# Performance work log

Hardware: AMD Instinct MI355X
Metric: run time of the kernel (lower is better)

Reference implementation:

```python
import jax, jax.numpy as jnp
import numpy as np

T = 2048      # number of utterances in the dialogue (sequential loop dim)
L = 50        # tokens per utterance
V = 30000     # vocab size
D = 300       # word embedding dim
NF = 64       # CNN filters per width
H = 100       # hidden size (hard-coded in CMN)
NC = 7        # emotion classes
WIND = 40     # args.wind1 sliding memory window
HOPS = 3      # args.hops
NEG = -1e10   # masked_fill value in dotprod_attention


def setup_inputs() -> dict:
    key = jax.random.key(0)
    ks = jax.random.split(key, 24)
    s = 0.05

    def n(k, shape):
        return jax.random.normal(k, shape, jnp.float32) * s

    return {
        "sents": jax.random.randint(ks[0], (T, L), 0, V, dtype=jnp.int32),
        "lengths": jax.random.randint(ks[1], (T,), 1, L, dtype=jnp.int32),
        "emb": n(ks[2], (V, D)),
        "Wc3": n(ks[3], (NF, 1, 3, D)), "bc3": n(ks[4], (NF,)),
        "Wc4": n(ks[5], (NF, 1, 4, D)), "bc4": n(ks[6], (NF,)),
        "Wc5": n(ks[7], (NF, 1, 5, D)), "bc5": n(ks[8], (NF,)),
        "Wt": n(ks[9], (3 * NF, H)), "bt": n(ks[10], (H,)),
        "Wih_c": n(ks[11], (3 * H, H)), "Whh_c": n(ks[12], (3 * H, H)),
        "bih_c": n(ks[13], (3 * H,)), "bhh_c": n(ks[14], (3 * H,)),
        "Wih_m": n(ks[15], (3 * H, H)), "Whh_m": n(ks[16], (3 * H, H)),
        "bih_m": n(ks[17], (3 * H,)), "bhh_m": n(ks[18], (3 * H,)),
        "Wcls": n(ks[19], (H, NC)), "bcls": n(ks[20], (NC,)),
    }


def _gru_cell(x, h, Wih, Whh, bih, bhh):
    # torch GRU cell, gate order (r, z, n)
    gi = x @ Wih.T + bih
    gh = h @ Whh.T + bhh
    ir, iz, inn = jnp.split(gi, 3, axis=-1)
    hr, hz, hn = jnp.split(gh, 3, axis=-1)
    r = jax.nn.sigmoid(ir + hr)
    z = jax.nn.sigmoid(iz + hz)
    nw = jnp.tanh(inn + r * hn)
    return (1.0 - z) * nw + z * h


def reference(sents, lengths, emb, Wc3, bc3, Wc4, bc4, Wc5, bc5, Wt, bt,
              Wih_c, Whh_c, bih_c, bhh_c, Wih_m, Whh_m, bih_m, bhh_m,
              Wcls, bcls):
    # ---- CNN utterance encoder (dropout layers are identity in eval) ----
    w = emb[sents]                       # (T, L, D)
    x = w[:, None]                       # (T, 1, L, D)  NCHW
    feats = []
    for Wc, bc in ((Wc3, bc3), (Wc4, bc4), (Wc5, bc5)):
        y = jax.lax.conv_general_dilated(
            x, Wc, window_strides=(1, 1), padding='VALID',
            dimension_numbers=('NCHW', 'OIHW', 'NCHW'))  # (T, NF, L-fs+1, 1)
        feats.append(jnp.max(jax.nn.relu(y + bc[None, :, None, None]), axis=(2, 3)))
    s_utt = jnp.tanh(jnp.concatenate(feats, axis=1) @ Wt + bt)  # (T, H)

    # ---- context GRU over utterances 0..T-2 (hidden after torch step i is hiddens[i-1]) ----
    def cont_step(h, u):
        h2 = _gru_cell(u, h, Wih_c, Whh_c, bih_c, bhh_c)
        return h2, h2
    _, hiddens = jax.lax.scan(cont_step, jnp.zeros((H,), jnp.float32), s_utt[:-1])  # (T-1, H)

    # ---- sliding memory windows: step i (1..T-1) sees hiddens[i-WIND .. i-1], newest last ----
    idx = jnp.arange(1, T)[:, None] - WIND + jnp.arange(WIND)[None, :]  # (T-1, WIND)
    valid = idx >= 0
    mem_all = jnp.where(valid[..., None], hiddens[jnp.clip(idx, 0)], 0.0)  # (T-1, WIND, H)

    def attend(query, mem, v):
        # query: (H,), mem: (WIND, H), v: (WIND,) bool
        for _ in range(HOPS):
            scores = jnp.where(v, mem @ query, NEG)
            a = jax.nn.softmax(scores)
            query = jnp.tanh(query + a @ mem)
            if HOPS > 1:
                # mem_gru over the valid suffix of the window (zero init hidden,
                # padded slots skipped so recurrence starts at first valid slot)
                def mstep(hm, xv):
                    xx, vv = xv
                    hn = _gru_cell(xx, hm, Wih_m, Whh_m, bih_m, bhh_m)
                    hm = jnp.where(vv, hn, hm)
                    return hm, hm
                _, mem = jax.lax.scan(mstep, jnp.zeros((H,), jnp.float32), (mem, v))
        return query

    queries = jax.vmap(attend)(s_utt[1:], mem_all, valid)       # (T-1, H)
    s_cont = jnp.concatenate([s_utt[:1], queries], axis=0)      # (T, H)
    logits = s_cont @ Wcls + bcls                                # (T, NC)
    return jax.nn.log_softmax(logits, axis=1)
```

## Files before the change

kernel.cpp:

```cpp
#include <hip/hip_runtime.h>

#define TT 2048
#define LL 50
#define DD 300
#define HH 100
#define NCC 7

typedef unsigned short u16;
typedef unsigned int u32;
typedef _Float16 f16x2 __attribute__((ext_vector_type(2)));
typedef _Float16 f16x4 __attribute__((ext_vector_type(4)));
typedef _Float16 f16x8 __attribute__((ext_vector_type(8)));
typedef float f32x4 __attribute__((ext_vector_type(4)));

__device__ __forceinline__ float frcp(float x){ return __builtin_amdgcn_rcpf(x); }
__device__ __forceinline__ float sigm(float x){ return frcp(1.f + __expf(-x)); }
__device__ __forceinline__ float ftanh(float x){ return 1.f - 2.f * frcp(1.f + __expf(2.f * x)); }

#if defined(__has_builtin)
#if __has_builtin(__builtin_amdgcn_fdot2)
#define HAS_FDOT2 1
#endif
#endif
__device__ __forceinline__ float fdot2(f16x2 a, f16x2 b, float c){
#ifdef HAS_FDOT2
  return __builtin_amdgcn_fdot2(a, b, c, false);
#else
  return c + (float)a.x * (float)b.x + (float)a.y * (float)b.y;
#endif
}
__device__ __forceinline__ f16x2 pk(float x, float y){ f16x2 r; r.x = (_Float16)x; r.y = (_Float16)y; return r; }

__global__ __launch_bounds__(256) void k_prep(const float* __restrict__ Wc3,
    const float* __restrict__ Wc4, const float* __restrict__ Wc5, _Float16* __restrict__ wtp)
{
  const int t = blockIdx.x;
  int kki, ntile, kt;
  if (t < 120){ kki = 0; ntile = t / 30;        kt = t % 30; }
  else if (t < 280){ kki = 1; int r = t - 120; ntile = r / 40; kt = r % 40; }
  else { kki = 2; int r = t - 280;             ntile = r / 50; kt = r % 50; }
  const float* W = (kki == 0) ? Wc3 : ((kki == 1) ? Wc4 : Wc5);
  const int kk = 3 + kki;
  #pragma unroll
  for (int u = 0; u < 2; ++u){
    int e = threadIdx.x * 2 + u;
    int lane = e >> 3, i = e & 7;
    int k = kt * 32 + (lane >> 4) * 8 + i;
    int f = ntile * 16 + (lane & 15);
    int j = k / 320, d = k - j * 320;
    float v = (d < DD) ? W[((size_t)f * kk + j) * DD + d] : 0.f;
    wtp[(size_t)t * 512 + e] = (_Float16)v;
  }
}

__global__ __launch_bounds__(256) void k_prep2(const float* __restrict__ Whh,
    const float* __restrict__ Wih, _Float16* __restrict__ wpkW, _Float16* __restrict__ wpkI)
{
  const float* W = (blockIdx.x == 0) ? Whh : Wih;
  _Float16* dst  = (blockIdx.x == 0) ? wpkW : wpkI;
  for (int idx = threadIdx.x; idx < 28 * 4 * 64 * 8; idx += 256){
    int i = idx & 7, lane = (idx >> 3) & 63, kt = (idx >> 9) & 3, mt = idx >> 11;
    int rl = lane & 15, gp = lane >> 4;
    int p = mt * 16 + rl;
    int k = kt * 32 + gp * 8 + i;
    int uu = p >> 2, g = p & 3;
    float v = (mt < 25 && g < 3 && k < 100) ? W[(size_t)(uu + 100 * g) * 100 + k] : 0.f;
    dst[idx] = (_Float16)v;
  }
}

#define WST 328
__global__ __launch_bounds__(256) void k_cnn(const int* __restrict__ sents,
    const float* __restrict__ emb, const _Float16* __restrict__ wtp,
    const float* __restrict__ bc3, const float* __restrict__ bc4, const float* __restrict__ bc5,
    const float* __restrict__ Wt,  const float* __restrict__ bt,
    float* __restrict__ su)
{
  __shared__ __attribute__((aligned(16))) _Float16 w16[52 * WST];
  __shared__ float feats[192];
  __shared__ int ids[LL];
  const int tid = threadIdx.x;
  const int s = blockIdx.x;

  if (tid < LL) ids[tid] = sents[s * LL + tid];
  for (int e = tid; e < 52 * WST / 2; e += 256) ((u32*)w16)[e] = 0u;
  __syncthreads();
  for (int e = tid; e < LL * 75; e += 256){
    int l = e / 75, d4 = (e - l * 75) * 4;
    float4 v = *(const float4*)&emb[(size_t)ids[l] * DD + d4];
    _Float16* p = &w16[l * WST + d4];
    p[0] = (_Float16)v.x; p[1] = (_Float16)v.y; p[2] = (_Float16)v.z; p[3] = (_Float16)v.w;
  }
  __syncthreads();

  const int lane = tid & 63, wid = tid >> 6;
  const int rl = lane & 15, gp = lane >> 4;
  const int kkstart[3] = {0, 120, 280};
  float fmaxv[3];
  #pragma unroll
  for (int kki = 0; kki < 3; ++kki){
    const int kk = 3 + kki, nkt = kk * 10, Pk = LL - kk + 1;
    f32x4 acc0 = {0.f,0.f,0.f,0.f}, acc1 = acc0, acc2 = acc0;
    const f16x8* bp = (const f16x8*)(wtp + (size_t)(kkstart[kki] + wid * nkt) * 512) + lane;
    int j = 0, d = gp * 8;
    for (int kt = 0; kt < nkt; ++kt){
      f16x8 b  = bp[(size_t)kt * 64];
      f16x8 a0 = *(const f16x8*)&w16[(rl      + j) * WST + d];
      f16x8 a1 = *(const f16x8*)&w16[(16 + rl + j) * WST + d];
      f16x8 a2 = *(const f16x8*)&w16[(32 + rl + j) * WST + d];
      acc0 = __builtin_amdgcn_mfma_f32_16x16x32_f16(a0, b, acc0, 0, 0, 0);
      acc1 = __builtin_amdgcn_mfma_f32_16x16x32_f16(a1, b, acc1, 0, 0, 0);
      acc2 = __builtin_amdgcn_mfma_f32_16x16x32_f16(a2, b, acc2, 0, 0, 0);
      d += 32; if (d >= 320){ d -= 320; ++j; }
    }
    float m = -1e30f;
    #pragma unroll
    for (int r = 0; r < 4; ++r){
      int p0 = gp * 4 + r;
      if (p0 < Pk)      m = fmaxf(m, acc0[r]);
      if (16 + p0 < Pk) m = fmaxf(m, acc1[r]);
      if (32 + p0 < Pk) m = fmaxf(m, acc2[r]);
    }
    m = fmaxf(m, __shfl_xor(m, 16));
    m = fmaxf(m, __shfl_xor(m, 32));
    fmaxv[kki] = m;
  }
  if (lane < 16){
    feats[  0 + wid * 16 + lane] = fmaxv[0];
    feats[ 64 + wid * 16 + lane] = fmaxv[1];
    feats[128 + wid * 16 + lane] = fmaxv[2];
  }
  __syncthreads();
  if (tid < 192){
    float bias = (tid < 64) ? bc3[tid] : ((tid < 128) ? bc4[tid - 64] : bc5[tid - 128]);
    feats[tid] = fmaxf(0.f, feats[tid] + bias);
  }
  __syncthreads();
  if (tid < HH){
    float acc = bt[tid];
    for (int c = 0; c < 192; ++c)
      acc += feats[c] * Wt[c * HH + tid];
    su[(size_t)s * HH + tid] = ftanh(acc);
  }
}

__global__ __launch_bounds__(320) void k_gi(const float* __restrict__ src,
    const float* __restrict__ W, const float* __restrict__ b, float* __restrict__ dst)
{
  __shared__ float x[HH];
  const int t = blockIdx.x, tid = threadIdx.x;
  if (tid < HH) x[tid] = src[(size_t)t * HH + tid];
  __syncthreads();
  if (tid < 300){
    float acc = b[tid];
    const float* wr = W + (size_t)tid * HH;
    #pragma unroll
    for (int i = 0; i < 25; ++i){
      float4 wv = *(const float4*)(wr + 4 * i);
      float4 xv = *(const float4*)&x[4 * i];
      acc += xv.x * wv.x + xv.y * wv.y + xv.z * wv.z + xv.w * wv.w;
    }
    dst[(size_t)t * 300 + tid] = acc;
  }
}

#define CH 32
__global__ __launch_bounds__(320, 1) void k_scan(const float* __restrict__ gi,
    const float* __restrict__ Whh, const float* __restrict__ bhh,
    float* __restrict__ hid, int steps)
{
  __shared__ __attribute__((aligned(16))) _Float16 h16[128];
  __shared__ __attribute__((aligned(16))) float gh_l[304];
  __shared__ float gi_buf[CH * 300];
  __shared__ float hid_buf[CH * HH];
  const int tid = threadIdx.x;
  const int lane = tid & 63, wvid = tid >> 6;
  const int rl = lane & 15, gp = lane >> 4;

  f16x8 afrag[4][4];
  #pragma unroll
  for (int m = 0; m < 4; ++m){
    int mt = wvid + 5 * m;
    int row = mt * 16 + rl;
    #pragma unroll
    for (int kt = 0; kt < 4; ++kt){
      f16x8 f;
      #pragma unroll
      for (int i = 0; i < 8; ++i){
        int k = kt * 32 + gp * 8 + i;
        float v = (row < 300 && k < 100) ? Whh[(size_t)row * 100 + k] : 0.f;
        f[i] = (_Float16)v;
      }
      afrag[m][kt] = f;
    }
  }
  float bhr = 0.f, bhz = 0.f, bhn = 0.f, hreg = 0.f;
  if (tid < HH){ bhr = bhh[tid]; bhz = bhh[tid + 100]; bhn = bhh[tid + 200]; }
  if (tid < 128) h16[tid] = (_Float16)0.f;
  {
    int c0 = (steps < CH ? steps : CH) * 75;
    for (int e = tid; e < c0; e += 320)
      ((float4*)gi_buf)[e] = ((const float4*)gi)[e];
  }
  __syncthreads();

  int t0 = 0;
  while (t0 < steps){
    int cnt = steps - t0; if (cnt > CH) cnt = CH;
    for (int s = 0; s < cnt; ++s){
      {
        const f16x8* hp = (const f16x8*)h16;
        f16x8 bf0 = hp[ 0 + gp], bf1 = hp[ 4 + gp], bf2 = hp[ 8 + gp], bf3 = hp[12 + gp];
        #pragma unroll
        for (int m = 0; m < 4; ++m){
          f32x4 acc = {0.f, 0.f, 0.f, 0.f};
          acc = __builtin_amdgcn_mfma_f32_16x16x32_f16(afrag[m][0], bf0, acc, 0, 0, 0);
          acc = __builtin_amdgcn_mfma_f32_16x16x32_f16(afrag[m][1], bf1, acc, 0, 0, 0);
          acc = __builtin_amdgcn_mfma_f32_16x16x32_f16(afrag[m][2], bf2, acc, 0, 0, 0);
          acc = __builtin_amdgcn_mfma_f32_16x16x32_f16(afrag[m][3], bf3, acc, 0, 0, 0);
          int mt = wvid + 5 * m;
          if (rl == 0 && mt < 19)
            *(float4*)&gh_l[mt * 16 + gp * 4] = *(float4*)&acc;
        }
      }
      __syncthreads();
      if (tid < HH){
        const float* gpp = gi_buf + s * 300;
        float r = sigm(gpp[tid]       + gh_l[tid]       + bhr);
        float z = sigm(gpp[tid + 100] + gh_l[tid + 100] + bhz);
        float n = ftanh(gpp[tid + 200] + r * (gh_l[tid + 200] + bhn));
        float o = (1.f - z) * n + z * hreg;
        hreg = o;
        h16[tid] = (_Float16)o;
        hid_buf[s * HH + tid] = o;
      }
      __syncthreads();
    }
    for (int e = tid; e < cnt * 25; e += 320)
      ((float4*)(hid + (size_t)t0 * HH))[e] = ((const float4*)hid_buf)[e];
    int nt0 = t0 + cnt;
    int ncnt = steps - nt0; if (ncnt > CH) ncnt = CH; if (ncnt < 0) ncnt = 0;
    for (int e = tid; e < ncnt * 75; e += 320)
      ((float4*)gi_buf)[e] = ((const float4*)(gi + (size_t)nt0 * 300))[e];
    __syncthreads();
    t0 = nt0;
  }
}

__global__ __launch_bounds__(256, 1) void k_att2(
    const float* __restrict__ su, const float* __restrict__ hid, const float* __restrict__ gm,
    const _Float16* __restrict__ wpkW, const _Float16* __restrict__ wpkI,
    const float* __restrict__ bih, const float* __restrict__ bhh,
    float* __restrict__ scont)
{
  __shared__ __attribute__((aligned(16))) _Float16 MEM[40][8][136];
  __shared__ __attribute__((aligned(16))) _Float16 H16[2][8][136];
  __shared__ __attribute__((aligned(16))) _Float16 GI2[8][8][100][4];
  __shared__ float QL[8][104];
  __shared__ float SC[8][40];

  const int tid = threadIdx.x;
  const int lane = tid & 63, wvid = tid >> 6;
  const int rl = lane & 15, gp = lane >> 4;
  const int qbase = blockIdx.x * 8;
  const int j = rl & 7;
  const int qi = qbase + j;
  int wminj = 39 - qi; if (wminj < 0) wminj = 0;
  if (qi >= TT - 1) wminj = 40;

  f16x8 aW[7][4];
  #pragma unroll
  for (int t = 0; t < 7; ++t){
    int mt = wvid + 4 * t;
    #pragma unroll
    for (int kt = 0; kt < 4; ++kt)
      aW[t][kt] = *(const f16x8*)(wpkW + (size_t)((mt * 4 + kt) * 64 + lane) * 8);
  }
  float bi_[7][3];
  #pragma unroll
  for (int t = 0; t < 7; ++t){
    int mt = wvid + 4 * t;
    bool v = (mt < 25);
    int uu = v ? (mt * 4 + gp) : 0;
    bi_[t][0] = v ? bih[uu]       : 0.f;
    bi_[t][1] = v ? bih[uu + 100] : 0.f;
    bi_[t][2] = v ? bih[uu + 200] : 0.f;
  }
  const int cbase = (rl < 8) ? 0 : 4;
  float bh_[4][3]; int cu[4]; bool cv[4];
  #pragma unroll
  for (int tt = 0; tt < 4; ++tt){
    int t = cbase + tt;
    int mt = wvid + 4 * t;
    bool v = (t < 7) && (mt < 25);
    cv[tt] = v;
    int uu = v ? (mt * 4 + gp) : 0;
    cu[tt] = uu;
    bh_[tt][0] = v ? bhh[uu]       : 0.f;
    bh_[tt][1] = v ? bhh[uu + 100] : 0.f;
    bh_[tt][2] = v ? bhh[uu + 200] : 0.f;
  }

  for (int e = tid; e < 40 * 8 * 34; e += 256){
    int i4 = e % 34, wj = e / 34, w = wj >> 3, jj = wj & 7;
    int qq = qbase + jj;
    int row = qq - 39 + w;
    f16x4 v4 = {0, 0, 0, 0};
    if (i4 < 25 && qq < TT - 1 && row >= 0){
      float4 f = *(const float4*)&hid[(size_t)row * HH + i4 * 4];
      v4[0] = (_Float16)f.x; v4[1] = (_Float16)f.y; v4[2] = (_Float16)f.z; v4[3] = (_Float16)f.w;
    }
    *(f16x4*)&MEM[w][jj][i4 * 4] = v4;
  }
  for (int e = tid; e < 8 * 104; e += 256){
    int jj = e / 104, ii = e % 104;
    int qq = qbase + jj;
    QL[jj][ii] = (ii < 100 && qq < TT - 1) ? su[(size_t)(qq + 1) * HH + ii] : 0.f;
  }
  for (int e = tid; e < 2 * 8 * 136; e += 256) ((_Float16*)H16)[e] = (_Float16)0;
  __syncthreads();

  for (int hop = 0; hop < 3; ++hop){
    for (int e = tid; e < 320; e += 256){
      int jj = e / 40, w = e % 40;
      int qq = qbase + jj;
      int wm = 39 - qq; if (wm < 0) wm = 0; if (qq >= TT - 1) wm = 40;
      float acc = 0.f;
      if (w >= wm){
        #pragma unroll
        for (int g = 0; g < 13; ++g){
          f16x8 m8 = *(const f16x8*)&MEM[w][jj][g * 8];
          const float* qp = &QL[jj][g * 8];
          #pragma unroll
          for (int i = 0; i < 8; ++i) acc += (float)m8[i] * qp[i];
        }
        SC[jj][w] = acc;
      } else SC[jj][w] = -1e10f;
    }
    __syncthreads();
    if (tid < 8){
      float m = -3e38f;
      for (int w = 0; w < 40; ++w) m = fmaxf(m, SC[tid][w]);
      float s = 0.f;
      for (int w = 0; w < 40; ++w){ float e = __expf(SC[tid][w] - m); SC[tid][w] = e; s += e; }
      float inv = frcp(s);
      for (int w = 0; w < 40; ++w) SC[tid][w] *= inv;
    }
    __syncthreads();
    for (int e = tid; e < 400; e += 256){
      int jj = e / 50, i2 = e % 50;
      float c0 = 0.f, c1 = 0.f;
      for (int w = 0; w < 40; ++w){
        float a = SC[jj][w];
        f16x2 m2 = *(const f16x2*)&MEM[w][jj][i2 * 2];
        c0 += a * (float)m2.x; c1 += a * (float)m2.y;
      }
      float q0 = ftanh(QL[jj][i2 * 2]     + c0);
      float q1 = ftanh(QL[jj][i2 * 2 + 1] + c1);
      QL[jj][i2 * 2] = q0; QL[jj][i2 * 2 + 1] = q1;
      if (hop == 2){
        int qq = qbase + jj;
        if (qq < TT - 1)
          *(float2*)&scont[(size_t)(qq + 1) * HH + i2 * 2] = make_float2(q0, q1);
      }
    }
    if (hop == 2) break;
    for (int e = tid; e < 800; e += 256) H16[0][e / 100][e % 100] = (_Float16)0;
    float hrg[4] = {0.f, 0.f, 0.f, 0.f};
    __syncthreads();

    for (int c = 0; c < 5; ++c){
      if (hop == 0){
        for (int e = tid; e < 6400; e += 256){
          int s8 = e / 800, jj = (e / 100) & 7, uu = e % 100;
          int qq = qbase + jj;
          int row = qq - 39 + c * 8 + s8;
          f16x4 g4 = {0, 0, 0, 0};
          if (qq < TT - 1 && row >= 0){
            const float* gr = &gm[(size_t)row * 300];
            g4[0] = (_Float16)gr[uu]; g4[1] = (_Float16)gr[uu + 100]; g4[2] = (_Float16)gr[uu + 200];
          }
          *(f16x4*)&GI2[s8][jj][uu][0] = g4;
        }
      } else {
        #pragma unroll
        for (int nt = 0; nt < 4; ++nt){
          f16x8 bf[4];
          #pragma unroll
          for (int kt = 0; kt < 4; ++kt)
            bf[kt] = *(const f16x8*)&MEM[c * 8 + nt * 2 + (rl >> 3)][rl & 7][kt * 32 + gp * 8];
          #pragma unroll
          for (int t = 0; t < 7; ++t){
            int mt = wvid + 4 * t;
            if (mt < 25){
              f32x4 ac = {0.f, 0.f, 0.f, 0.f};
              #pragma unroll
              for (int kt = 0; kt < 4; ++kt){
                f16x8 ai = *(const f16x8*)(wpkI + (size_t)((mt * 4 + kt) * 64 + lane) * 8);
                ac = __builtin_amdgcn_mfma_f32_16x16x32_f16(ai, bf[kt], ac, 0, 0, 0);
              }
              int uu = mt * 4 + gp;
              int s8 = nt * 2 + (rl >> 3), jj = rl & 7;
              f16x4 g4;
              g4[0] = (_Float16)(ac[0] + bi_[t][0]);
              g4[1] = (_Float16)(ac[1] + bi_[t][1]);
              g4[2] = (_Float16)(ac[2] + bi_[t][2]);
              g4[3] = (_Float16)0.f;
              *(f16x4*)&GI2[s8][jj][uu][0] = g4;
            }
          }
        }
      }
      __syncthreads();
      for (int s = 0; s < 8; ++s){
        int w = c * 8 + s;
        const _Float16 (*hs)[136] = H16[w & 1];
        _Float16 (*hd)[136] = H16[(w + 1) & 1];
        f16x8 b0 = *(const f16x8*)&hs[j][      gp * 8];
        f16x8 b1 = *(const f16x8*)&hs[j][32  + gp * 8];
        f16x8 b2 = *(const f16x8*)&hs[j][64  + gp * 8];
        f16x8 b3 = *(const f16x8*)&hs[j][96  + gp * 8];
        f32x4 acc[7];
        #pragma unroll
        for (int t = 0; t < 7; ++t){
          int mt = wvid + 4 * t;
          f32x4 a = {0.f, 0.f, 0.f, 0.f};
          if (mt < 25){
            a = __builtin_amdgcn_mfma_f32_16x16x32_f16(aW[t][0], b0, a, 0, 0, 0);
            a = __builtin_amdgcn_mfma_f32_16x16x32_f16(aW[t][1], b1, a, 0, 0, 0);
            a = __builtin_amdgcn_mfma_f32_16x16x32_f16(aW[t][2], b2, a, 0, 0, 0);
            a = __builtin_amdgcn_mfma_f32_16x16x32_f16(aW[t][3], b3, a, 0, 0, 0);
          }
          acc[t] = a;
        }
        const bool vw = (w >= wminj);
        #pragma unroll
        for (int tt = 0; tt < 4; ++tt){
          if (cv[tt]){
            f32x4 ac = (rl < 8) ? acc[tt] : acc[(tt + 4 < 7) ? (tt + 4) : 6];
            f16x4 g4 = *(const f16x4*)&GI2[s][j][cu[tt]][0];
            float r = sigm((float)g4[0] + ac[0] + bh_[tt][0]);
            float z = sigm((float)g4[1] + ac[1] + bh_[tt][1]);
            float n = ftanh((float)g4[2] + r * (ac[2] + bh_[tt][2]));
            float o = vw ? ((1.f - z) * n + z * hrg[tt]) : hrg[tt];
            hrg[tt] = o;
            hd[j][cu[tt]]     = (_Float16)o;
            MEM[w][j][cu[tt]] = (_Float16)o;
          }
        }
        __syncthreads();
      }
    }
  }
}

__global__ __launch_bounds__(256) void k_cls(const float* __restrict__ su, const float* __restrict__ scont,
    const float* __restrict__ Wcls, const float* __restrict__ bcls, float* __restrict__ out)
{
  __shared__ float wl[HH * NCC];
  __shared__ float bl[NCC];
  const int tid = threadIdx.x;
  for (int e = tid; e < HH * NCC; e += 256) wl[e] = Wcls[e];
  if (tid < NCC) bl[tid] = bcls[tid];
  __syncthreads();
  int r = blockIdx.x * 256 + tid;
  if (r < TT){
    const float* v = (r == 0) ? su : (scont + (size_t)r * HH);
    float l[NCC];
    #pragma unroll
    for (int c = 0; c < NCC; ++c) l[c] = bl[c];
    for (int h = 0; h < HH; ++h){
      float x = v[h];
      #pragma unroll
      for (int c = 0; c < NCC; ++c) l[c] += x * wl[h * NCC + c];
    }
    float m = l[0];
    #pragma unroll
    for (int c = 1; c < NCC; ++c) m = fmaxf(m, l[c]);
    float ssum = 0.f;
    #pragma unroll
    for (int c = 0; c < NCC; ++c) ssum += __expf(l[c] - m);
    float lse = m + __logf(ssum);
    #pragma unroll
    for (int c = 0; c < NCC; ++c) out[(size_t)r * NCC + c] = l[c] - lse;
  }
}

extern "C" void kernel_launch(void* const* d_in, const int* in_sizes, int n_in,
                              void* d_out, int out_size, void* d_ws, size_t ws_size,
                              hipStream_t stream)
{
  const int* sents  = (const int*)d_in[0];
  const float* emb    = (const float*)d_in[2];
  const float* Wc3    = (const float*)d_in[3];  const float* bc3 = (const float*)d_in[4];
  const float* Wc4    = (const float*)d_in[5];  const float* bc4 = (const float*)d_in[6];
  const float* Wc5    = (const float*)d_in[7];  const float* bc5 = (const float*)d_in[8];
  const float* Wt     = (const float*)d_in[9];  const float* bt  = (const float*)d_in[10];
  const float* Wih_c  = (const float*)d_in[11]; const float* Whh_c = (const float*)d_in[12];
  const float* bih_c  = (const float*)d_in[13]; const float* bhh_c = (const float*)d_in[14];
  const float* Wih_m  = (const float*)d_in[15]; const float* Whh_m = (const float*)d_in[16];
  const float* bih_m  = (const float*)d_in[17]; const float* bhh_m = (const float*)d_in[18];
  const float* Wcls   = (const float*)d_in[19]; const float* bcls  = (const float*)d_in[20];

  float* ws    = (float*)d_ws;
  float* su    = ws;
  float* gic   = su  + 204800;
  float* hid   = gic + 614100;
  float* gm    = gic;
  float* scont = hid + 204700;
  _Float16* wtp  = (_Float16*)(scont + 204800);
  _Float16* wpkW = wtp + 245760;
  _Float16* wpkI = wpkW + 57344;

  k_prep <<<480,    256, 0, stream>>>(Wc3, Wc4, Wc5, wtp);
  k_prep2<<<2,      256, 0, stream>>>(Whh_m, Wih_m, wpkW, wpkI);
  k_cnn  <<<TT,     256, 0, stream>>>(sents, emb, wtp, bc3, bc4, bc5, Wt, bt, su);
  k_gi   <<<TT - 1, 320, 0, stream>>>(su, Wih_c, bih_c, gic);
  k_scan <<<1,      320, 0, stream>>>(gic, Whh_c, bhh_c, hid, TT - 1);
  k_gi   <<<TT - 1, 320, 0, stream>>>(hid, Wih_m, bih_m, gm);
  k_att2 <<<256,    256, 0, stream>>>(su, hid, gm, wpkW, wpkI, bih_m, bhh_m, scont);
  k_cls  <<<(TT + 255) / 256, 256, 0, stream>>>(su, scont, Wcls, bcls, (float*)d_out);
}
```

Baseline: 1.744 ms.

## Fuse CNN, GRU scan, attention and classifier into one persistent flag-synchronized kernel

Merges the CNN encoder, input-gate projection, sequential context GRU scan, memory attention and classifier into a single persistent kernel of 256 blocks. Block 0 runs the scan and consumes per-utterance flags published by the other blocks. Once the scan progress counter passes their queries, all blocks run attention. The attention's hop-0 input projection is now computed in-kernel with MFMA instead of a separate k_gi pass, and the classifier is folded into the attention tail. This is meant to overlap CNN work with the serial scan and remove launch and global round-trip costs, at the price of spin-wait synchronization and a dependency on all 256 blocks being co-resident.

```diff
diff --git a/kernel.cpp b/kernel.cpp
--- a/kernel.cpp
+++ b/kernel.cpp
@@ -17,19 +17,12 @@
 __device__ __forceinline__ float sigm(float x){ return frcp(1.f + __expf(-x)); }
 __device__ __forceinline__ float ftanh(float x){ return 1.f - 2.f * frcp(1.f + __expf(2.f * x)); }
 
-#if defined(__has_builtin)
-#if __has_builtin(__builtin_amdgcn_fdot2)
-#define HAS_FDOT2 1
-#endif
-#endif
-__device__ __forceinline__ float fdot2(f16x2 a, f16x2 b, float c){
-#ifdef HAS_FDOT2
-  return __builtin_amdgcn_fdot2(a, b, c, false);
-#else
-  return c + (float)a.x * (float)b.x + (float)a.y * (float)b.y;
-#endif
-}
-__device__ __forceinline__ f16x2 pk(float x, float y){ f16x2 r; r.x = (_Float16)x; r.y = (_Float16)y; return r; }
+__device__ __forceinline__ int ld_acq(int* p){
+  return __hip_atomic_load(p, __ATOMIC_ACQUIRE, __HIP_MEMORY_SCOPE_AGENT);
+}
+__device__ __forceinline__ void st_rel(int* p, int v){
+  __hip_atomic_store(p, v, __ATOMIC_RELEASE, __HIP_MEMORY_SCOPE_AGENT);
+}
 
 __global__ __launch_bounds__(256) void k_prep(const float* __restrict__ Wc3,
     const float* __restrict__ Wc4, const float* __restrict__ Wc5, _Float16* __restrict__ wtp)
@@ -69,200 +62,248 @@
   }
 }
 
+__global__ __launch_bounds__(256) void k_zero(int* __restrict__ flags)
+{
+  int i = blockIdx.x * 256 + threadIdx.x;
+  if (i < 2049) flags[i] = 0;
+}
+
 #define WST 328
-__global__ __launch_bounds__(256) void k_cnn(const int* __restrict__ sents,
-    const float* __restrict__ emb, const _Float16* __restrict__ wtp,
+#define CH 32
+__global__ __launch_bounds__(256, 1) void k_mega(
+    const int* __restrict__ sents, const float* __restrict__ emb, const _Float16* __restrict__ wtp,
     const float* __restrict__ bc3, const float* __restrict__ bc4, const float* __restrict__ bc5,
     const float* __restrict__ Wt,  const float* __restrict__ bt,
-    float* __restrict__ su)
+    const float* __restrict__ Wih_c, const float* __restrict__ bih_c,
+    const float* __restrict__ Whh_c, const float* __restrict__ bhh_c,
+    const _Float16* __restrict__ wpkW, const _Float16* __restrict__ wpkI,
+    const float* __restrict__ bih_m, const float* __restrict__ bhh_m,
+    const float* __restrict__ Wcls, const float* __restrict__ bcls,
+    float* __restrict__ su, float* __restrict__ gic, float* __restrict__ hid,
+    int* __restrict__ flags, float* __restrict__ out)
 {
-  __shared__ __attribute__((aligned(16))) _Float16 w16[52 * WST];
-  __shared__ float feats[192];
-  __shared__ int ids[LL];
+  __shared__ __attribute__((aligned(16))) char smem[147456];
   const int tid = threadIdx.x;
-  const int s = blockIdx.x;
-
-  if (tid < LL) ids[tid] = sents[s * LL + tid];
-  for (int e = tid; e < 52 * WST / 2; e += 256) ((u32*)w16)[e] = 0u;
-  __syncthreads();
-  for (int e = tid; e < LL * 75; e += 256){
-    int l = e / 75, d4 = (e - l * 75) * 4;
-    float4 v = *(const float4*)&emb[(size_t)ids[l] * DD + d4];
-    _Float16* p = &w16[l * WST + d4];
-    p[0] = (_Float16)v.x; p[1] = (_Float16)v.y; p[2] = (_Float16)v.z; p[3] = (_Float16)v.w;
-  }
-  __syncthreads();
-
-  const int lane = tid & 63, wid = tid >> 6;
-  const int rl = lane & 15, gp = lane >> 4;
-  const int kkstart[3] = {0, 120, 280};
-  float fmaxv[3];
-  #pragma unroll
-  for (int kki = 0; kki < 3; ++kki){
-    const int kk = 3 + kki, nkt = kk * 10, Pk = LL - kk + 1;
-    f32x4 acc0 = {0.f,0.f,0.f,0.f}, acc1 = acc0, acc2 = acc0;
-    const f16x8* bp = (const f16x8*)(wtp + (size_t)(kkstart[kki] + wid * nkt) * 512) + lane;
-    int j = 0, d = gp * 8;
-    for (int kt = 0; kt < nkt; ++kt){
-      f16x8 b  = bp[(size_t)kt * 64];
-      f16x8 a0 = *(const f16x8*)&w16[(rl      + j) * WST + d];
-      f16x8 a1 = *(const f16x8*)&w16[(16 + rl + j) * WST + d];
-      f16x8 a2 = *(const f16x8*)&w16[(32 + rl + j) * WST + d];
-      acc0 = __builtin_amdgcn_mfma_f32_16x16x32_f16(a0, b, acc0, 0, 0, 0);
-      acc1 = __builtin_amdgcn_mfma_f32_16x16x32_f16(a1, b, acc1, 0, 0, 0);
-      acc2 = __builtin_amdgcn_mfma_f32_16x16x32_f16(a2, b, acc2, 0, 0, 0);
-      d += 32; if (d >= 320){ d -= 320; ++j; }
-    }
-    float m = -1e30f;
-    #pragma unroll
-    for (int r = 0; r < 4; ++r){
-      int p0 = gp * 4 + r;
-      if (p0 < Pk)      m = fmaxf(m, acc0[r]);
-      if (16 + p0 < Pk) m = fmaxf(m, acc1[r]);
-      if (32 + p0 < Pk) m = fmaxf(m, acc2[r]);
-    }
-    m = fmaxf(m, __shfl_xor(m, 16));
-    m = fmaxf(m, __shfl_xor(m, 32));
-    fmaxv[kki] = m;
-  }
-  if (lane < 16){
-    feats[  0 + wid * 16 + lane] = fmaxv[0];
-    feats[ 64 + wid * 16 + lane] = fmaxv[1];
-    feats[128 + wid * 16 + lane] = fmaxv[2];
-  }
-  __syncthreads();
-  if (tid < 192){
-    float bias = (tid < 64) ? bc3[tid] : ((tid < 128) ? bc4[tid - 64] : bc5[tid - 128]);
-    feats[tid] = fmaxf(0.f, feats[tid] + bias);
-  }
-  __syncthreads();
-  if (tid < HH){
-    float acc = bt[tid];
-    for (int c = 0; c < 192; ++c)
-      acc += feats[c] * Wt[c * HH + tid];
-    su[(size_t)s * HH + tid] = ftanh(acc);
-  }
-}
-
-__global__ __launch_bounds__(320) void k_gi(const float* __restrict__ src,
-    const float* __restrict__ W, const float* __restrict__ b, float* __restrict__ dst)
-{
-  __shared__ float x[HH];
-  const int t = blockIdx.x, tid = threadIdx.x;
-  if (tid < HH) x[tid] = src[(size_t)t * HH + tid];
-  __syncthreads();
-  if (tid < 300){
-    float acc = b[tid];
-    const float* wr = W + (size_t)tid * HH;
-    #pragma unroll
-    for (int i = 0; i < 25; ++i){
-      float4 wv = *(const float4*)(wr + 4 * i);
-      float4 xv = *(const float4*)&x[4 * i];
-      acc += xv.x * wv.x + xv.y * wv.y + xv.z * wv.z + xv.w * wv.w;
-    }
-    dst[(size_t)t * 300 + tid] = acc;
-  }
-}
-
-#define CH 32
-__global__ __launch_bounds__(320, 1) void k_scan(const float* __restrict__ gi,
-    const float* __restrict__ Whh, const float* __restrict__ bhh,
-    float* __restrict__ hid, int steps)
-{
-  __shared__ __attribute__((aligned(16))) _Float16 h16[128];
-  __shared__ __attribute__((aligned(16))) float gh_l[304];
-  __shared__ float gi_buf[CH * 300];
-  __shared__ float hid_buf[CH * HH];
-  const int tid = threadIdx.x;
+  const int b = blockIdx.x;
   const int lane = tid & 63, wvid = tid >> 6;
   const int rl = lane & 15, gp = lane >> 4;
 
-  f16x8 afrag[4][4];
-  #pragma unroll
-  for (int m = 0; m < 4; ++m){
-    int mt = wvid + 5 * m;
-    int row = mt * 16 + rl;
+  if (b > 0){
+    _Float16* w16 = (_Float16*)smem;
+    float* feats  = (float*)(smem + 34112);
+    int*   ids    = (int*)(smem + 34880);
+    float* su_l   = (float*)(smem + 35088);
+
+    for (int s = b - 1; s < TT; s += 255){
+      if (tid < LL) ids[tid] = sents[s * LL + tid];
+      for (int e = tid; e < 52 * WST / 2; e += 256) ((u32*)w16)[e] = 0u;
+      __syncthreads();
+      for (int e = tid; e < LL * 75; e += 256){
+        int l = e / 75, d4 = (e - l * 75) * 4;
+        float4 v = *(const float4*)&emb[(size_t)ids[l] * DD + d4];
+        _Float16* p = &w16[l * WST + d4];
+        p[0] = (_Float16)v.x; p[1] = (_Float16)v.y; p[2] = (_Float16)v.z; p[3] = (_Float16)v.w;
+      }
+      __syncthreads();
+
+      const int kkstart[3] = {0, 120, 280};
+      float fmaxv[3];
+      #pragma unroll
+      for (int kki = 0; kki < 3; ++kki){
+        const int nkt = (3 + kki) * 10, Pk = LL - (3 + kki) + 1;
+        f32x4 acc0 = {0.f,0.f,0.f,0.f}, acc1 = acc0, acc2 = acc0;
+        const f16x8* bp = (const f16x8*)(wtp + (size_t)(kkstart[kki] + wvid * nkt) * 512) + lane;
+        int j = 0, d = gp * 8;
+        for (int kt = 0; kt < nkt; ++kt){
+          f16x8 bb = bp[(size_t)kt * 64];
+          f16x8 a0 = *(const f16x8*)&w16[(rl      + j) * WST + d];
+          f16x8 a1 = *(const f16x8*)&w16[(16 + rl + j) * WST + d];
+          f16x8 a2 = *(const f16x8*)&w16[(32 + rl + j) * WST + d];
+          acc0 = __builtin_amdgcn_mfma_f32_16x16x32_f16(a0, bb, acc0, 0, 0, 0);
+          acc1 = __builtin_amdgcn_mfma_f32_16x16x32_f16(a1, bb, acc1, 0, 0, 0);
+          acc2 = __builtin_amdgcn_mfma_f32_16x16x32_f16(a2, bb, acc2, 0, 0, 0);
+          d += 32; if (d >= 320){ d -= 320; ++j; }
+        }
+        float m = -1e30f;
+        #pragma unroll
+        for (int r = 0; r < 4; ++r){
+          int p0 = gp * 4 + r;
+          if (p0 < Pk)      m = fmaxf(m, acc0[r]);
+          if (16 + p0 < Pk) m = fmaxf(m, acc1[r]);
+          if (32 + p0 < Pk) m = fmaxf(m, acc2[r]);
+        }
+        m = fmaxf(m, __shfl_xor(m, 16));
+        m = fmaxf(m, __shfl_xor(m, 32));
+        fmaxv[kki] = m;
+      }
+      if (lane < 16){
+        feats[  0 + wvid * 16 + lane] = fmaxv[0];
+        feats[ 64 + wvid * 16 + lane] = fmaxv[1];
+        feats[128 + wvid * 16 + lane] = fmaxv[2];
+      }
+      __syncthreads();
+      if (tid < 192){
+        float bias = (tid < 64) ? bc3[tid] : ((tid < 128) ? bc4[tid - 64] : bc5[tid - 128]);
+        feats[tid] = fmaxf(0.f, feats[tid] + bias);
+      }
+      __syncthreads();
+      if (tid < HH){
+        float acc = bt[tid];
+        for (int c = 0; c < 192; ++c)
+          acc += feats[c] * Wt[c * HH + tid];
+        float v = ftanh(acc);
+        su[(size_t)s * HH + tid] = v;
+        su_l[tid] = v;
+      }
+      __syncthreads();
+      if (s < TT - 1){
+        for (int e = tid; e < 300; e += 256){
+          const float* wr = Wih_c + (size_t)e * 100;
+          float acc = bih_c[e];
+          #pragma unroll
+          for (int i = 0; i < 25; ++i){
+            float4 wv = *(const float4*)(wr + 4 * i);
+            float4 xv = *(const float4*)&su_l[4 * i];
+            acc += xv.x * wv.x + xv.y * wv.y + xv.z * wv.z + xv.w * wv.w;
+          }
+          gic[(size_t)s * 300 + e] = acc;
+        }
+      }
+      __syncthreads();
+      if (tid == 0){ __threadfence(); st_rel(&flags[s], 1); }
+    }
+  } else {
+    _Float16* h16  = (_Float16*)smem;
+    float* gh_l    = (float*)(smem + 256);
+    float* gi_buf  = (float*)(smem + 1472);
+    float* hid_buf = (float*)(smem + 39872);
+    const int steps = TT - 1;
+
+    f16x8 afrag[5][4];
     #pragma unroll
-    for (int kt = 0; kt < 4; ++kt){
-      f16x8 f;
+    for (int m = 0; m < 5; ++m){
+      int mt = wvid + 4 * m;
+      int row = mt * 16 + rl;
       #pragma unroll
-      for (int i = 0; i < 8; ++i){
-        int k = kt * 32 + gp * 8 + i;
-        float v = (row < 300 && k < 100) ? Whh[(size_t)row * 100 + k] : 0.f;
-        f[i] = (_Float16)v;
-      }
-      afrag[m][kt] = f;
-    }
-  }
-  float bhr = 0.f, bhz = 0.f, bhn = 0.f, hreg = 0.f;
-  if (tid < HH){ bhr = bhh[tid]; bhz = bhh[tid + 100]; bhn = bhh[tid + 200]; }
-  if (tid < 128) h16[tid] = (_Float16)0.f;
-  {
-    int c0 = (steps < CH ? steps : CH) * 75;
-    for (int e = tid; e < c0; e += 320)
-      ((float4*)gi_buf)[e] = ((const float4*)gi)[e];
-  }
+      for (int kt = 0; kt < 4; ++kt){
+        f16x8 f;
+        #pragma unroll
+        for (int i = 0; i < 8; ++i){
+          int k = kt * 32 + gp * 8 + i;
+          float v = (row < 300 && k < 100) ? Whh_c[(size_t)row * 100 + k] : 0.f;
+          f[i] = (_Float16)v;
+        }
+        afrag[m][kt] = f;
+      }
+    }
+    float bhr = 0.f, bhz = 0.f, bhn = 0.f, hreg = 0.f;
+    if (tid < HH){ bhr = bhh_c[tid]; bhz = bhh_c[tid + 100]; bhn = bhh_c[tid + 200]; }
+    if (tid < 128) h16[tid] = (_Float16)0.f;
+    {
+      int n0 = steps < CH ? steps : CH;
+      for (int e = tid; e < n0; e += 256)
+        while (!ld_acq(&flags[e])) __builtin_amdgcn_s_sleep(2);
+    }
+    __syncthreads();
+    {
+      int c0 = (steps < CH ? steps : CH) * 75;
+      for (int e = tid; e < c0; e += 256)
+        ((float4*)gi_buf)[e] = ((const float4*)gic)[e];
+    }
+    __syncthreads();
+
+    int t0 = 0;
+    while (t0 < steps){
+      int cnt = steps - t0; if (cnt > CH) cnt = CH;
+      for (int s = 0; s < cnt; ++s){
+        {
+          const f16x8* hp = (const f16x8*)h16;
+          f16x8 bf0 = hp[0 + gp], bf1 = hp[4 + gp], bf2 = hp[8 + gp], bf3 = hp[12 + gp];
+          #pragma unroll
+          for (int m = 0; m < 5; ++m){
+            f32x4 acc = {0.f, 0.f, 0.f, 0.f};
+            acc = __builtin_amdgcn_mfma_f32_16x16x32_f16(afrag[m][0], bf0, acc, 0, 0, 0);
+            acc = __builtin_amdgcn_mfma_f32_16x16x32_f16(afrag[m][1], bf1, acc, 0, 0, 0);
+            acc = __builtin_amdgcn_mfma_f32_16x16x32_f16(afrag[m][2], bf2, acc, 0, 0, 0);
+            acc = __builtin_amdgcn_mfma_f32_16x16x32_f16(afrag[m][3], bf3, acc, 0, 0, 0);
+            int mt = wvid + 4 * m;
+            if (rl == 0 && mt < 19)
+              *(float4*)&gh_l[mt * 16 + gp * 4] = *(float4*)&acc;
+          }
+        }
+        __syncthreads();
+        if (tid < HH){
+          const float* gpp = gi_buf + s * 300;
+          float r = sigm(gpp[tid]       + gh_l[tid]       + bhr);
+          float z = sigm(gpp[tid + 100] + gh_l[tid + 100] + bhz);
+          float n = ftanh(gpp[tid + 200] + r * (gh_l[tid + 200] + bhn));
+          float o = (1.f - z) * n + z * hreg;
+          hreg = o;
+          h16[tid] = (_Float16)o;
+          hid_buf[s * HH + tid] = o;
+        }
+        __syncthreads();
+      }
+      for (int e = tid; e < cnt * 25; e += 256)
+        ((float4*)(hid + (size_t)t0 * HH))[e] = ((const float4*)hid_buf)[e];
+      int nt0 = t0 + cnt;
+      int ncnt = steps - nt0; if (ncnt > CH) ncnt = CH; if (ncnt < 0) ncnt = 0;
+      for (int e = tid; e < ncnt; e += 256)
+        while (!ld_acq(&flags[nt0 + e])) __builtin_amdgcn_s_sleep(2);
+      __syncthreads();
+      if (tid == 0){ __threadfence(); st_rel(&flags[2048], nt0); }
+      for (int e = tid; e < ncnt * 75; e += 256)
+        ((float4*)gi_buf)[e] = ((const float4*)(gic + (size_t)nt0 * 300))[e];
+      __syncthreads();
+      t0 = nt0;
+    }
+  }
+
   __syncthreads();
-
-  int t0 = 0;
-  while (t0 < steps){
-    int cnt = steps - t0; if (cnt > CH) cnt = CH;
-    for (int s = 0; s < cnt; ++s){
-      {
-        const f16x8* hp = (const f16x8*)h16;
-        f16x8 bf0 = hp[ 0 + gp], bf1 = hp[ 4 + gp], bf2 = hp[ 8 + gp], bf3 = hp[12 + gp];
-        #pragma unroll
-        for (int m = 0; m < 4; ++m){
-          f32x4 acc = {0.f, 0.f, 0.f, 0.f};
-          acc = __builtin_amdgcn_mfma_f32_16x16x32_f16(afrag[m][0], bf0, acc, 0, 0, 0);
-          acc = __builtin_amdgcn_mfma_f32_16x16x32_f16(afrag[m][1], bf1, acc, 0, 0, 0);
-          acc = __builtin_amdgcn_mfma_f32_16x16x32_f16(afrag[m][2], bf2, acc, 0, 0, 0);
-          acc = __builtin_amdgcn_mfma_f32_16x16x32_f16(afrag[m][3], bf3, acc, 0, 0, 0);
-          int mt = wvid + 5 * m;
-          if (rl == 0 && mt < 19)
-            *(float4*)&gh_l[mt * 16 + gp * 4] = *(float4*)&acc;
-        }
-      }
-      __syncthreads();
-      if (tid < HH){
-        const float* gpp = gi_buf + s * 300;
-        float r = sigm(gpp[tid]       + gh_l[tid]       + bhr);
-        float z = sigm(gpp[tid + 100] + gh_l[tid + 100] + bhz);
-        float n = ftanh(gpp[tid + 200] + r * (gh_l[tid + 200] + bhn));
-        float o = (1.f - z) * n + z * hreg;
-        hreg = o;
-        h16[tid] = (_Float16)o;
-        hid_buf[s * HH + tid] = o;
-      }
-      __syncthreads();
-    }
-    for (int e = tid; e < cnt * 25; e += 320)
-      ((float4*)(hid + (size_t)t0 * HH))[e] = ((const float4*)hid_buf)[e];
-    int nt0 = t0 + cnt;
-    int ncnt = steps - nt0; if (ncnt > CH) ncnt = CH; if (ncnt < 0) ncnt = 0;
-    for (int e = tid; e < ncnt * 75; e += 320)
-      ((float4*)gi_buf)[e] = ((const float4*)(gi + (size_t)nt0 * 300))[e];
-    __syncthreads();
-    t0 = nt0;
-  }
-}
-
-__global__ __launch_bounds__(256, 1) void k_att2(
-    const float* __restrict__ su, const float* __restrict__ hid, const float* __restrict__ gm,
-    const _Float16* __restrict__ wpkW, const _Float16* __restrict__ wpkI,
-    const float* __restrict__ bih, const float* __restrict__ bhh,
-    float* __restrict__ scont)
-{
-  __shared__ __attribute__((aligned(16))) _Float16 MEM[40][8][136];
-  __shared__ __attribute__((aligned(16))) _Float16 H16[2][8][136];
-  __shared__ __attribute__((aligned(16))) _Float16 GI2[8][8][100][4];
-  __shared__ float QL[8][104];
-  __shared__ float SC[8][40];
-
-  const int tid = threadIdx.x;
-  const int lane = tid & 63, wvid = tid >> 6;
-  const int rl = lane & 15, gp = lane >> 4;
-  const int qbase = blockIdx.x * 8;
+  const int grp = (b == 0) ? 255 : (b - 1);
+  const int qbase = grp * 8;
+  if (tid < 8){
+    int qq = qbase + tid;
+    if (qq < TT - 1)
+      while (!ld_acq(&flags[qq + 1])) __builtin_amdgcn_s_sleep(8);
+  }
+  if (tid == 1){
+    int need = qbase + 8; if (need > TT - 1) need = TT - 1;
+    while (ld_acq(&flags[2048]) < need) __builtin_amdgcn_s_sleep(32);
+  }
+  if (b == 0 && tid == 0){
+    while (!ld_acq(&flags[0])) __builtin_amdgcn_s_sleep(2);
+    float l[NCC];
+    #pragma unroll
+    for (int c = 0; c < NCC; ++c) l[c] = bcls[c];
+    for (int h = 0; h < HH; ++h){
+      float x = su[h];
+      #pragma unroll
+      for (int c = 0; c < NCC; ++c) l[c] += x * Wcls[h * NCC + c];
+    }
+    float m = l[0];
+    #pragma unroll
+    for (int c = 1; c < NCC; ++c) m = fmaxf(m, l[c]);
+    float ssum = 0.f;
+    #pragma unroll
+    for (int c = 0; c < NCC; ++c) ssum += __expf(l[c] - m);
+    float lse = m + __logf(ssum);
+    #pragma unroll
+    for (int c = 0; c < NCC; ++c) out[c] = l[c] - lse;
+  }
+  __syncthreads();
+
+  _Float16* MEMb = (_Float16*)smem;
+  _Float16* H16b = (_Float16*)(smem + 87040);
+  _Float16* GI2b = (_Float16*)(smem + 91392);
+  float* QLb     = (float*)(smem + 142592);
+  float* SCb     = (float*)(smem + 145920);
+  #define MEM_(w,j,i)   MEMb[((w)*8+(j))*136 + (i)]
+  #define H16_(d,j,i)   H16b[((d)*8+(j))*136 + (i)]
+  #define GI2_(s,j,u)   GI2b[(((s)*8+(j))*100 + (u))*4]
+  #define QL_(j,i)      QLb[(j)*104 + (i)]
+  #define SC_(j,w)      SCb[(j)*40 + (w)]
+
   const int j = rl & 7;
   const int qi = qbase + j;
   int wminj = 39 - qi; if (wminj < 0) wminj = 0;
@@ -282,9 +323,9 @@
     int mt = wvid + 4 * t;
     bool v = (mt < 25);
     int uu = v ? (mt * 4 + gp) : 0;
-    bi_[t][0] = v ? bih[uu]       : 0.f;
-    bi_[t][1] = v ? bih[uu + 100] : 0.f;
-    bi_[t][2] = v ? bih[uu + 200] : 0.f;
+    bi_[t][0] = v ? bih_m[uu]       : 0.f;
+    bi_[t][1] = v ? bih_m[uu + 100] : 0.f;
+    bi_[t][2] = v ? bih_m[uu + 200] : 0.f;
   }
   const int cbase = (rl < 8) ? 0 : 4;
   float bh_[4][3]; int cu[4]; bool cv[4];
@@ -296,9 +337,9 @@
     cv[tt] = v;
     int uu = v ? (mt * 4 + gp) : 0;
     cu[tt] = uu;
-    bh_[tt][0] = v ? bhh[uu]       : 0.f;
-    bh_[tt][1] = v ? bhh[uu + 100] : 0.f;
-    bh_[tt][2] = v ? bhh[uu + 200] : 0.f;
+    bh_[tt][0] = v ? bhh_m[uu]       : 0.f;
+    bh_[tt][1] = v ? bhh_m[uu + 100] : 0.f;
+    bh_[tt][2] = v ? bhh_m[uu + 200] : 0.f;
   }
 
   for (int e = tid; e < 40 * 8 * 34; e += 256){
@@ -310,14 +351,14 @@
       float4 f = *(const float4*)&hid[(size_t)row * HH + i4 * 4];
       v4[0] = (_Float16)f.x; v4[1] = (_Float16)f.y; v4[2] = (_Float16)f.z; v4[3] = (_Float16)f.w;
     }
-    *(f16x4*)&MEM[w][jj][i4 * 4] = v4;
+    *(f16x4*)&MEM_(w, jj, i4 * 4) = v4;
   }
   for (int e = tid; e < 8 * 104; e += 256){
     int jj = e / 104, ii = e % 104;
     int qq = qbase + jj;
-    QL[jj][ii] = (ii < 100 && qq < TT - 1) ? su[(size_t)(qq + 1) * HH + ii] : 0.f;
-  }
-  for (int e = tid; e < 2 * 8 * 136; e += 256) ((_Float16*)H16)[e] = (_Float16)0;
+    QL_(jj, ii) = (ii < 100 && qq < TT - 1) ? su[(size_t)(qq + 1) * HH + ii] : 0.f;
+  }
+  for (int e = tid; e < 2 * 8 * 136; e += 256) H16b[e] = (_Float16)0;
   __syncthreads();
 
   for (int hop = 0; hop < 3; ++hop){
@@ -325,101 +366,103 @@
       int jj = e / 40, w = e % 40;
       int qq = qbase + jj;
       int wm = 39 - qq; if (wm < 0) wm = 0; if (qq >= TT - 1) wm = 40;
-      float acc = 0.f;
       if (w >= wm){
+        float acc = 0.f;
         #pragma unroll
         for (int g = 0; g < 13; ++g){
-          f16x8 m8 = *(const f16x8*)&MEM[w][jj][g * 8];
-          const float* qp = &QL[jj][g * 8];
+          f16x8 m8 = *(const f16x8*)&MEM_(w, jj, g * 8);
+          const float* qp = &QL_(jj, g * 8);
           #pragma unroll
           for (int i = 0; i < 8; ++i) acc += (float)m8[i] * qp[i];
         }
-        SC[jj][w] = acc;
-      } else SC[jj][w] = -1e10f;
+        SC_(jj, w) = acc;
+      } else SC_(jj, w) = -1e10f;
     }
     __syncthreads();
     if (tid < 8){
       float m = -3e38f;
-      for (int w = 0; w < 40; ++w) m = fmaxf(m, SC[tid][w]);
+      for (int w = 0; w < 40; ++w) m = fmaxf(m, SC_(tid, w));
       float s = 0.f;
-      for (int w = 0; w < 40; ++w){ float e = __expf(SC[tid][w] - m); SC[tid][w] = e; s += e; }
+      for (int w = 0; w < 40; ++w){ float e = __expf(SC_(tid, w) - m); SC_(tid, w) = e; s += e; }
       float inv = frcp(s);
-      for (int w = 0; w < 40; ++w) SC[tid][w] *= inv;
+      for (int w = 0; w < 40; ++w) SC_(tid, w) *= inv;
     }
     __syncthreads();
     for (int e = tid; e < 400; e += 256){
       int jj = e / 50, i2 = e % 50;
       float c0 = 0.f, c1 = 0.f;
       for (int w = 0; w < 40; ++w){
-        float a = SC[jj][w];
-        f16x2 m2 = *(const f16x2*)&MEM[w][jj][i2 * 2];
+        float a = SC_(jj, w);
+        f16x2 m2 = *(const f16x2*)&MEM_(w, jj, i2 * 2);
         c0 += a * (float)m2.x; c1 += a * (float)m2.y;
       }
-      float q0 = ftanh(QL[jj][i2 * 2]     + c0);
-      float q1 = ftanh(QL[jj][i2 * 2 + 1] + c1);
-      QL[jj][i2 * 2] = q0; QL[jj][i2 * 2 + 1] = q1;
-      if (hop == 2){
-        int qq = qbase + jj;
-        if (qq < TT - 1)
-          *(float2*)&scont[(size_t)(qq + 1) * HH + i2 * 2] = make_float2(q0, q1);
-      }
-    }
-    if (hop == 2) break;
-    for (int e = tid; e < 800; e += 256) H16[0][e / 100][e % 100] = (_Float16)0;
+      QL_(jj, i2 * 2)     = ftanh(QL_(jj, i2 * 2)     + c0);
+      QL_(jj, i2 * 2 + 1) = ftanh(QL_(jj, i2 * 2 + 1) + c1);
+    }
+    if (hop == 2){
+      __syncthreads();
+      for (int e = tid; e < 56; e += 256){
+        int jj = e / 7, c = e % 7;
+        float lg = bcls[c];
+        for (int h = 0; h < HH; ++h) lg += QL_(jj, h) * Wcls[h * NCC + c];
+        SC_(jj, c) = lg;
+      }
+      __syncthreads();
+      if (tid < 8){
+        int qq = qbase + tid;
+        if (qq < TT - 1){
+          float m = SC_(tid, 0);
+          #pragma unroll
+          for (int c = 1; c < NCC; ++c) m = fmaxf(m, SC_(tid, c));
+          float ssum = 0.f;
+          #pragma unroll
+          for (int c = 0; c < NCC; ++c) ssum += __expf(SC_(tid, c) - m);
+          float lse = m + __logf(ssum);
+          #pragma unroll
+          for (int c = 0; c < NCC; ++c) out[(size_t)(qq + 1) * NCC + c] = SC_(tid, c) - lse;
+        }
+      }
+      break;
+    }
+    for (int e = tid; e < 800; e += 256) H16_(0, e / 100, e % 100) = (_Float16)0;
     float hrg[4] = {0.f, 0.f, 0.f, 0.f};
     __syncthreads();
 
     for (int c = 0; c < 5; ++c){
-      if (hop == 0){
-        for (int e = tid; e < 6400; e += 256){
-          int s8 = e / 800, jj = (e / 100) & 7, uu = e % 100;
-          int qq = qbase + jj;
-          int row = qq - 39 + c * 8 + s8;
-          f16x4 g4 = {0, 0, 0, 0};
-          if (qq < TT - 1 && row >= 0){
-            const float* gr = &gm[(size_t)row * 300];
-            g4[0] = (_Float16)gr[uu]; g4[1] = (_Float16)gr[uu + 100]; g4[2] = (_Float16)gr[uu + 200];
-          }
-          *(f16x4*)&GI2[s8][jj][uu][0] = g4;
-        }
-      } else {
-        #pragma unroll
-        for (int nt = 0; nt < 4; ++nt){
-          f16x8 bf[4];
-          #pragma unroll
-          for (int kt = 0; kt < 4; ++kt)
-            bf[kt] = *(const f16x8*)&MEM[c * 8 + nt * 2 + (rl >> 3)][rl & 7][kt * 32 + gp * 8];
-          #pragma unroll
-          for (int t = 0; t < 7; ++t){
-            int mt = wvid + 4 * t;
-            if (mt < 25){
-              f32x4 ac = {0.f, 0.f, 0.f, 0.f};
-              #pragma unroll
-              for (int kt = 0; kt < 4; ++kt){
-                f16x8 ai = *(const f16x8*)(wpkI + (size_t)((mt * 4 + kt) * 64 + lane) * 8);
-                ac = __builtin_amdgcn_mfma_f32_16x16x32_f16(ai, bf[kt], ac, 0, 0, 0);
-              }
-              int uu = mt * 4 + gp;
-              int s8 = nt * 2 + (rl >> 3), jj = rl & 7;
-              f16x4 g4;
-              g4[0] = (_Float16)(ac[0] + bi_[t][0]);
-              g4[1] = (_Float16)(ac[1] + bi_[t][1]);
-              g4[2] = (_Float16)(ac[2] + bi_[t][2]);
-              g4[3] = (_Float16)0.f;
-              *(f16x4*)&GI2[s8][jj][uu][0] = g4;
+      #pragma unroll
+      for (int nt = 0; nt < 4; ++nt){
+        f16x8 bf[4];
+        #pragma unroll
+        for (int kt = 0; kt < 4; ++kt)
+          bf[kt] = *(const f16x8*)&MEM_(c * 8 + nt * 2 + (rl >> 3), rl & 7, kt * 32 + gp * 8);
+        #pragma unroll
+        for (int t = 0; t < 7; ++t){
+          int mt = wvid + 4 * t;
+          if (mt < 25){
+            f32x4 ac = {0.f, 0.f, 0.f, 0.f};
+            #pragma unroll
+            for (int kt = 0; kt < 4; ++kt){
+              f16x8 ai = *(const f16x8*)(wpkI + (size_t)((mt * 4 + kt) * 64 + lane) * 8);
+              ac = __builtin_amdgcn_mfma_f32_16x16x32_f16(ai, bf[kt], ac, 0, 0, 0);
             }
+            int uu = mt * 4 + gp;
+            int s8 = nt * 2 + (rl >> 3), jj = rl & 7;
+            f16x4 g4;
+            g4[0] = (_Float16)(ac[0] + bi_[t][0]);
+            g4[1] = (_Float16)(ac[1] + bi_[t][1]);
+            g4[2] = (_Float16)(ac[2] + bi_[t][2]);
+            g4[3] = (_Float16)0.f;
+            *(f16x4*)&GI2_(s8, jj, uu) = g4;
           }
         }
       }
       __syncthreads();
       for (int s = 0; s < 8; ++s){
         int w = c * 8 + s;
-        const _Float16 (*hs)[136] = H16[w & 1];
-        _Float16 (*hd)[136] = H16[(w + 1) & 1];
-        f16x8 b0 = *(const f16x8*)&hs[j][      gp * 8];
-        f16x8 b1 = *(const f16x8*)&hs[j][32  + gp * 8];
-        f16x8 b2 = *(const f16x8*)&hs[j][64  + gp * 8];
-        f16x8 b3 = *(const f16x8*)&hs[j][96  + gp * 8];
+        f16x8 b0 = *(const f16x8*)&H16_(w & 1, j,       gp * 8);
+        f16x8 b1 = *(const f16x8*)&H16_(w & 1, j, 32  + gp * 8);
+        f16x8 b2 = *(const f16x8*)&H16_(w & 1, j, 64  + gp * 8);
+        f16x8 b3 = *(const f16x8*)&H16_(w & 1, j, 96  + gp * 8);
         f32x4 acc[7];
         #pragma unroll
         for (int t = 0; t < 7; ++t){
@@ -438,52 +481,25 @@
         for (int tt = 0; tt < 4; ++tt){
           if (cv[tt]){
             f32x4 ac = (rl < 8) ? acc[tt] : acc[(tt + 4 < 7) ? (tt + 4) : 6];
-            f16x4 g4 = *(const f16x4*)&GI2[s][j][cu[tt]][0];
+            f16x4 g4 = *(const f16x4*)&GI2_(s, j, cu[tt]);
             float r = sigm((float)g4[0] + ac[0] + bh_[tt][0]);
             float z = sigm((float)g4[1] + ac[1] + bh_[tt][1]);
             float n = ftanh((float)g4[2] + r * (ac[2] + bh_[tt][2]));
             float o = vw ? ((1.f - z) * n + z * hrg[tt]) : hrg[tt];
             hrg[tt] = o;
-            hd[j][cu[tt]]     = (_Float16)o;
-            MEM[w][j][cu[tt]] = (_Float16)o;
+            H16_((w + 1) & 1, j, cu[tt]) = (_Float16)o;
+            MEM_(w, j, cu[tt]) = (_Float16)o;
           }
         }
         __syncthreads();
       }
     }
   }
-}
-
-__global__ __launch_bounds__(256) void k_cls(const float* __restrict__ su, const float* __restrict__ scont,
-    const float* __restrict__ Wcls, const float* __restrict__ bcls, float* __restrict__ out)
-{
-  __shared__ float wl[HH * NCC];
-  __shared__ float bl[NCC];
-  const int tid = threadIdx.x;
-  for (int e = tid; e < HH * NCC; e += 256) wl[e] = Wcls[e];
-  if (tid < NCC) bl[tid] = bcls[tid];
-  __syncthreads();
-  int r = blockIdx.x * 256 + tid;
-  if (r < TT){
-    const float* v = (r == 0) ? su : (scont + (size_t)r * HH);
-    float l[NCC];
-    #pragma unroll
-    for (int c = 0; c < NCC; ++c) l[c] = bl[c];
-    for (int h = 0; h < HH; ++h){
-      float x = v[h];
-      #pragma unroll
-      for (int c = 0; c < NCC; ++c) l[c] += x * wl[h * NCC + c];
-    }
-    float m = l[0];
-    #pragma unroll
-    for (int c = 1; c < NCC; ++c) m = fmaxf(m, l[c]);
-    float ssum = 0.f;
-    #pragma unroll
-    for (int c = 0; c < NCC; ++c) ssum += __expf(l[c] - m);
-    float lse = m + __logf(ssum);
-    #pragma unroll
-    for (int c = 0; c < NCC; ++c) out[(size_t)r * NCC + c] = l[c] - lse;
-  }
+  #undef MEM_
+  #undef H16_
+  #undef GI2_
+  #undef QL_
+  #undef SC_
 }
 
 extern "C" void kernel_launch(void* const* d_in, const int* in_sizes, int n_in,
@@ -506,18 +522,16 @@
   float* su    = ws;
   float* gic   = su  + 204800;
   float* hid   = gic + 614100;
-  float* gm    = gic;
-  float* scont = hid + 204700;
-  _Float16* wtp  = (_Float16*)(scont + 204800);
+  _Float16* wtp  = (_Float16*)(hid + 204700);
   _Float16* wpkW = wtp + 245760;
   _Float16* wpkI = wpkW + 57344;
-
-  k_prep <<<480,    256, 0, stream>>>(Wc3, Wc4, Wc5, wtp);
-  k_prep2<<<2,      256, 0, stream>>>(Whh_m, Wih_m, wpkW, wpkI);
-  k_cnn  <<<TT,     256, 0, stream>>>(sents, emb, wtp, bc3, bc4, bc5, Wt, bt, su);
-  k_gi   <<<TT - 1, 320, 0, stream>>>(su, Wih_c, bih_c, gic);
-  k_scan <<<1,      320, 0, stream>>>(gic, Whh_c, bhh_c, hid, TT - 1);
-  k_gi   <<<TT - 1, 320, 0, stream>>>(hid, Wih_m, bih_m, gm);
-  k_att2 <<<256,    256, 0, stream>>>(su, hid, gm, wpkW, wpkI, bih_m, bhh_m, scont);
-  k_cls  <<<(TT + 255) / 256, 256, 0, stream>>>(su, scont, Wcls, bcls, (float*)d_out);
-}
+  int* flags     = (int*)(wpkI + 57344);
+
+  k_prep <<<480, 256, 0, stream>>>(Wc3, Wc4, Wc5, wtp);
+  k_prep2<<<2,   256, 0, stream>>>(Whh_m, Wih_m, wpkW, wpkI);
+  k_zero <<<9,   256, 0, stream>>>(flags);
+  k_mega <<<256, 256, 0, stream>>>(sents, emb, wtp, bc3, bc4, bc5, Wt, bt,
+                                   Wih_c, bih_c, Whh_c, bhh_c,
+                                   wpkW, wpkI, bih_m, bhh_m, Wcls, bcls,
+                                   su, gic, hid, flags, (float*)d_out);
+}
```

Measured after the change: 1.881 ms. +7.8%, slower.
